# Kernel optimization log

Measured on AMD Instinct MI355X. Metric: run time of the kernel, lower is better.

Reference implementation:

```python
import jax, jax.numpy as jnp
import numpy as np

N_NODES = 50000
N_EDGES = 800000
IN_CH, HID, OUT_CH = 3, 64, 768
NEG_SLOPE = 0.01  # torch LeakyReLU default
BN_EPS = 1e-5


def _gcn_conv(x, edge_index, W, b):
    # PyG GCNConv: add self-loops, symmetric degree normalization, scatter-add.
    n = x.shape[0]
    loops = jnp.arange(n, dtype=edge_index.dtype)
    src = jnp.concatenate([edge_index[0], loops])
    dst = jnp.concatenate([edge_index[1], loops])
    deg = jax.ops.segment_sum(jnp.ones(src.shape[0], x.dtype), dst, num_segments=n)
    dinv = jnp.where(deg > 0, jax.lax.rsqrt(deg), 0.0)
    norm = dinv[src] * dinv[dst]                      # [E+N]
    h = x @ W                                          # [N, out]
    msg = h[src] * norm[:, None]                       # gather + edge scale
    return jax.ops.segment_sum(msg, dst, num_segments=n) + b


def _block(x, edge_index, W, b, gamma, beta):
    h = _gcn_conv(x, edge_index, W, b)
    h = jnp.where(h >= 0, h, NEG_SLOPE * h)            # LeakyReLU
    mean = h.mean(axis=0)
    var = h.var(axis=0)                                # biased, as torch BN train
    h = (h - mean) * jax.lax.rsqrt(var + BN_EPS) * gamma + beta
    return h                                           # dropout: identity (eval)


def _glorot(key, fan_in, fan_out):
    s = np.sqrt(6.0 / (fan_in + fan_out)).astype(np.float32)
    return jax.random.uniform(key, (fan_in, fan_out), jnp.float32, -s, s)


def setup_inputs() -> dict:
    key = jax.random.key(0)
    ks = jax.random.split(key, 8)
    x = jax.random.normal(ks[0], (N_NODES, IN_CH), jnp.float32)
    edge_index = jax.random.randint(ks[1], (2, N_EDGES), 0, N_NODES, jnp.int64)
    inp = {"x": x, "edge_index": edge_index}
    inp["W1"] = _glorot(ks[2], IN_CH, HID)
    inp["b1"] = jnp.zeros((HID,), jnp.float32)
    inp["g1"] = jnp.ones((HID,), jnp.float32)
    inp["be1"] = jnp.zeros((HID,), jnp.float32)
    inp["W2"] = _glorot(ks[3], HID, HID)
    inp["b2"] = jnp.zeros((HID,), jnp.float32)
    inp["g2"] = jnp.ones((HID,), jnp.float32)
    inp["be2"] = jnp.zeros((HID,), jnp.float32)
    inp["W3"] = _glorot(ks[4], HID, HID)
    inp["b3"] = jnp.zeros((HID,), jnp.float32)
    inp["g3"] = jnp.ones((HID,), jnp.float32)
    inp["be3"] = jnp.zeros((HID,), jnp.float32)
    inp["Wmu"] = _glorot(ks[5], HID, OUT_CH)
    inp["bmu"] = jnp.zeros((OUT_CH,), jnp.float32)
    inp["Wls"] = _glorot(ks[6], HID, OUT_CH)
    inp["bls"] = jnp.zeros((OUT_CH,), jnp.float32)
    return inp


def reference(x, edge_index, W1, b1, g1, be1, W2, b2, g2, be2, W3, b3, g3, be3, Wmu, bmu, Wls, bls):
    h = _block(x, edge_index, W1, b1, g1, be1)
    h = _block(h, edge_index, W2, b2, g2, be2)
    h = _block(h, edge_index, W3, b3, g3, be3)
    mu = _gcn_conv(h, edge_index, Wmu, bmu)
    logstd = _gcn_conv(h, edge_index, Wls, bls)
    return (mu, logstd)
```

## Files before the change

### kernel.cpp

```cpp
#include <hip/hip_runtime.h>
#include <cstddef>


#define NEG_SLOPE 0.01f
#define BN_EPS 1e-5f

typedef unsigned short u16;
typedef __attribute__((ext_vector_type(8))) short bf16x8;
typedef __attribute__((ext_vector_type(4))) float f32x4;

__device__ __forceinline__ unsigned bf16_rne(float x) {
  unsigned u = __float_as_uint(x);
  return (u + 0x7fffu + ((u >> 16) & 1u)) >> 16;
}

__global__ __launch_bounds__(256) void init_k(int* __restrict__ cnt,
                                              float* __restrict__ bns, int N) {
  int i = blockIdx.x * 256 + threadIdx.x;
  if (i < N) cnt[i] = 0;
  if (i < 384) bns[i] = 0.0f;
}

__global__ __launch_bounds__(256) void hist_k(const int* __restrict__ dst,
                                              int* __restrict__ cnt, int E) {
  int e = blockIdx.x * 256 + threadIdx.x;
  if (e < E) atomicAdd(&cnt[dst[e]], 1);
}

__global__ __launch_bounds__(1024) void scanA(const int* __restrict__ cnt,
                                              int* __restrict__ pre,
                                              int* __restrict__ bsum, int N) {
  __shared__ int sh[1024];
  const int t = threadIdx.x;
  const int i = blockIdx.x * 1024 + t;
  int c = (i < N) ? cnt[i] : 0;
  sh[t] = c;
  __syncthreads();
  for (int off = 1; off < 1024; off <<= 1) {
    int v = (t >= off) ? sh[t - off] : 0;
    __syncthreads();
    sh[t] += v;
    __syncthreads();
  }
  if (i < N) pre[i] = sh[t] - c;
  if (t == 1023) bsum[blockIdx.x] = sh[t];
}

__global__ __launch_bounds__(64) void scanB(int* __restrict__ bsum, int nb) {
  int t = threadIdx.x;
  int orig = (t < nb) ? bsum[t] : 0;
  int v = orig;
#pragma unroll
  for (int off = 1; off < 64; off <<= 1) {
    int u = __shfl_up(v, off);
    if (t >= off) v += u;
  }
  if (t < nb) bsum[t] = v - orig;
}

__global__ __launch_bounds__(256) void scanC(const int* __restrict__ cnt,
                                             int* __restrict__ rowptr,
                                             int* __restrict__ cursor,
                                             const int* __restrict__ bsum,
                                             const float* __restrict__ x,
                                             float* __restrict__ dinv,
                                             float4* __restrict__ xd,
                                             int N, int E) {
  int i = blockIdx.x * 256 + threadIdx.x;
  if (i < N) {
    int rp = rowptr[i] + bsum[i >> 10];
    rowptr[i] = rp;
    cursor[i] = rp;
    float dv = rsqrtf((float)(cnt[i] + 1));
    dinv[i] = dv;
    xd[i] = make_float4(x[i * 3] * dv, x[i * 3 + 1] * dv, x[i * 3 + 2] * dv, dv);
  }
  if (i == 0) rowptr[N] = E;
}

__global__ __launch_bounds__(256) void fill_k(const int* __restrict__ src,
                                              const int* __restrict__ dst,
                                              int* __restrict__ cursor,
                                              int* __restrict__ eidx, int E) {
  int e = blockIdx.x * 256 + threadIdx.x;
  if (e >= E) return;
  int p = atomicAdd(&cursor[dst[e]], 1);
  eidx[p] = src[e];
}

__global__ __launch_bounds__(256) void l1_fused(
    const int* __restrict__ rowptr, const int* __restrict__ eidx,
    const float4* __restrict__ xd, const float* __restrict__ W1,
    const float* __restrict__ b1, float* __restrict__ Z, float* __restrict__ q,
    float* __restrict__ bns, int N) {
  const int t = threadIdx.x, lane = t & 63, wid = t >> 6;
  const int gw = blockIdx.x * 4 + wid;
  const int nw = gridDim.x * 4;
  const float w0 = W1[lane], w1 = W1[64 + lane], w2 = W1[128 + lane];
  const float bb = b1[lane];
  float s1 = 0.f, s2 = 0.f;
  for (int node = gw; node < N; node += nw) {
    int beg = rowptr[node], end = rowptr[node + 1];
    float a0 = 0.f, a1 = 0.f, a2 = 0.f, aq = 0.f;
    for (int e = beg + lane; e < end; e += 64) {
      float4 v = xd[eidx[e]];
      a0 += v.x;
      a1 += v.y;
      a2 += v.z;
      aq += v.w;
    }
#pragma unroll
    for (int off = 32; off; off >>= 1) {
      a0 += __shfl_xor(a0, off);
      a1 += __shfl_xor(a1, off);
      a2 += __shfl_xor(a2, off);
      aq += __shfl_xor(aq, off);
    }
    float4 sv = xd[node];
    float dv = sv.w;
    a0 += sv.x;
    a1 += sv.y;
    a2 += sv.z;
    aq += dv;
    float u = dv * (a0 * w0 + a1 * w1 + a2 * w2) + bb;
    float o = u >= 0.f ? u : NEG_SLOPE * u;
    Z[(size_t)node * 64 + lane] = o * dv;
    s1 += o;
    s2 += o * o;
    if (lane == 0) q[node] = aq;
  }
  __shared__ float red[8][64];
  red[wid][lane] = s1;
  red[4 + wid][lane] = s2;
  __syncthreads();
  if (t < 64) {
    atomicAdd(&bns[t], red[0][t] + red[1][t] + red[2][t] + red[3][t]);
    atomicAdd(&bns[64 + t], red[4][t] + red[5][t] + red[6][t] + red[7][t]);
  }
}

__global__ __launch_bounds__(256) void gather64(const int* __restrict__ rowptr,
                                                const int* __restrict__ eidx,
                                                const float* __restrict__ Z,
                                                float* __restrict__ G, int N) {
  int node = blockIdx.x * 4 + (threadIdx.x >> 6);
  if (node >= N) return;
  int lane = threadIdx.x & 63;
  int slot = lane >> 4;
  int c4 = (lane & 15) << 2;
  int beg = rowptr[node], end = rowptr[node + 1];
  float ax = 0.f, ay = 0.f, az = 0.f, aw = 0.f;
  int e = beg + slot;
  for (; e + 4 < end; e += 8) {
    int s0 = eidx[e], s1 = eidx[e + 4];
    float4 v0 = *(const float4*)(Z + (size_t)s0 * 64 + c4);
    float4 v1 = *(const float4*)(Z + (size_t)s1 * 64 + c4);
    ax += v0.x + v1.x;
    ay += v0.y + v1.y;
    az += v0.z + v1.z;
    aw += v0.w + v1.w;
  }
  if (e < end) {
    int s0 = eidx[e];
    float4 v0 = *(const float4*)(Z + (size_t)s0 * 64 + c4);
    ax += v0.x; ay += v0.y; az += v0.z; aw += v0.w;
  }
#pragma unroll
  for (int off = 16; off < 64; off <<= 1) {
    ax += __shfl_xor(ax, off);
    ay += __shfl_xor(ay, off);
    az += __shfl_xor(az, off);
    aw += __shfl_xor(aw, off);
  }
  if (slot == 0) {
    float4 self = *(const float4*)(Z + (size_t)node * 64 + c4);
    float4 o = make_float4(ax + self.x, ay + self.y, az + self.z, aw + self.w);
    *(float4*)(G + (size_t)node * 64 + c4) = o;
  }
}

__global__ __launch_bounds__(256) void gather64h(const int* __restrict__ rowptr,
                                                 const int* __restrict__ eidx,
                                                 const float* __restrict__ Z,
                                                 u16* __restrict__ Ghi,
                                                 u16* __restrict__ Glo, int N) {
  int node = blockIdx.x * 4 + (threadIdx.x >> 6);
  if (node >= N) return;
  int lane = threadIdx.x & 63;
  int slot = lane >> 4;
  int c4 = (lane & 15) << 2;
  int beg = rowptr[node], end = rowptr[node + 1];
  float ax = 0.f, ay = 0.f, az = 0.f, aw = 0.f;
  int e = beg + slot;
  for (; e + 4 < end; e += 8) {
    int s0 = eidx[e], s1 = eidx[e + 4];
    float4 v0 = *(const float4*)(Z + (size_t)s0 * 64 + c4);
    float4 v1 = *(const float4*)(Z + (size_t)s1 * 64 + c4);
    ax += v0.x + v1.x;
    ay += v0.y + v1.y;
    az += v0.z + v1.z;
    aw += v0.w + v1.w;
  }
  if (e < end) {
    int s0 = eidx[e];
    float4 v0 = *(const float4*)(Z + (size_t)s0 * 64 + c4);
    ax += v0.x; ay += v0.y; az += v0.z; aw += v0.w;
  }
#pragma unroll
  for (int off = 16; off < 64; off <<= 1) {
    ax += __shfl_xor(ax, off);
    ay += __shfl_xor(ay, off);
    az += __shfl_xor(az, off);
    aw += __shfl_xor(aw, off);
  }
  if (slot == 0) {
    float4 self = *(const float4*)(Z + (size_t)node * 64 + c4);
    float o0 = ax + self.x, o1 = ay + self.y, o2 = az + self.z, o3 = aw + self.w;
    unsigned h0 = bf16_rne(o0), h1 = bf16_rne(o1), h2 = bf16_rne(o2), h3 = bf16_rne(o3);
    unsigned l0 = bf16_rne(o0 - __uint_as_float(h0 << 16));
    unsigned l1 = bf16_rne(o1 - __uint_as_float(h1 << 16));
    unsigned l2 = bf16_rne(o2 - __uint_as_float(h2 << 16));
    unsigned l3 = bf16_rne(o3 - __uint_as_float(h3 << 16));
    uint2 hv = make_uint2(h0 | (h1 << 16), h2 | (h3 << 16));
    uint2 lv = make_uint2(l0 | (l1 << 16), l2 | (l3 << 16));
    *(uint2*)(Ghi + (size_t)node * 64 + c4) = hv;
    *(uint2*)(Glo + (size_t)node * 64 + c4) = lv;
  }
}

__global__ __launch_bounds__(256) void prep_head(
    const float* __restrict__ bns, const float* __restrict__ g,
    const float* __restrict__ be, const float* __restrict__ Wmu,
    const float* __restrict__ Wls, u16* __restrict__ Bh, u16* __restrict__ Bl,
    float* __restrict__ cmu, float* __restrict__ cls, float invN) {
  __shared__ float sc[64], sh[64], part[2][128];
  int t = threadIdx.x;
  if (t < 64) {
    float mean = bns[t] * invN;
    float var = bns[64 + t] * invN - mean * mean;
    float s = g[t] * rsqrtf(var + BN_EPS);
    sc[t] = s;
    sh[t] = be[t] - mean * s;
  }
  __syncthreads();
  int blk = blockIdx.x;
  int head = blk >= 6 ? 1 : 0;
  int cc = head ? blk - 6 : blk;
  int c0 = cc * 128;
  const float* W = head ? Wls : Wmu;
  float* cx = head ? cls : cmu;
  int cl = t & 127, kh = t >> 7;
  int c = c0 + cl;
  int ct = cl >> 4, jc = cl & 15;
  size_t base = (size_t)(head * 6 + cc) * 2 * 8 * 64 * 8;
  float p = 0.f;
  for (int k = kh * 32; k < kh * 32 + 32; ++k) {
    float w = W[(size_t)k * 768 + c];
    float wc = sc[k] * w;
    p += sh[k] * w;
    unsigned hi = bf16_rne(wc);
    unsigned lo = bf16_rne(wc - __uint_as_float(hi << 16));
    int lane = ((k >> 3) & 3) * 16 + jc;
    size_t idx = base + (((size_t)kh * 8 + ct) * 64 + lane) * 8 + (k & 7);
    Bh[idx] = (u16)hi;
    Bl[idx] = (u16)lo;
  }
  part[kh][cl] = p;
  __syncthreads();
  if (t < 128) cx[c0 + t] = part[0][t] + part[1][t];
}

__global__ __launch_bounds__(256, 4) void gemm_bnq2(
    const float* __restrict__ G, const float* __restrict__ dinv,
    const float* __restrict__ q, const float* __restrict__ W,
    const float* __restrict__ g, const float* __restrict__ be,
    const float* __restrict__ bnsPrev, const float* __restrict__ b,
    float* __restrict__ Z, float* __restrict__ bnsOut, float invN, int N) {
  __shared__ __align__(16) float P[64][68];
  __shared__ __align__(16) float Ws[64][64];
  __shared__ float scl[64], shl[64], cxl[64], part[4][64];
  const int t = threadIdx.x;
  const int r0 = blockIdx.x * 64;

  if (t < 64) {
    float mean = bnsPrev[t] * invN;
    float var = bnsPrev[64 + t] * invN - mean * mean;
    float s = g[t] * rsqrtf(var + BN_EPS);
    scl[t] = s;
    shl[t] = be[t] - mean * s;
  }
  for (int i = t; i < 1024; i += 256) {
    int r = i >> 4, k4 = (i & 15) << 2, gr = r0 + r;
    float4 v = make_float4(0.f, 0.f, 0.f, 0.f);
    if (gr < N) v = *(const float4*)(G + (size_t)gr * 64 + k4);
    *(float4*)&P[r][k4] = v;
  }
  for (int i = t; i < 4096; i += 256) Ws[i >> 6][i & 63] = W[i];
  __syncthreads();

  {
    const int c = t & 63, k0 = t >> 6;
    float p = 0.f;
#pragma unroll
    for (int s = 0; s < 16; ++s) {
      int k = k0 + (s << 2);
      float w = Ws[k][c];
      Ws[k][c] = scl[k] * w;
      p += shl[k] * w;
    }
    part[k0][c] = p;
  }
  __syncthreads();
  if (t < 64) cxl[t] = part[0][t] + part[1][t] + part[2][t] + part[3][t];
  __syncthreads();

  const int tr = t >> 4, tc4 = (t & 15) << 2;
  float acc[4][4] = {};
#pragma unroll 8
  for (int k = 0; k < 64; ++k) {
    float4 w = *(const float4*)&Ws[k][tc4];
#pragma unroll
    for (int i = 0; i < 4; ++i) {
      float a = P[tr + 16 * i][k];
      acc[i][0] += a * w.x;
      acc[i][1] += a * w.y;
      acc[i][2] += a * w.z;
      acc[i][3] += a * w.w;
    }
  }

  float s1[4] = {0.f, 0.f, 0.f, 0.f}, s2[4] = {0.f, 0.f, 0.f, 0.f};
  float4 bb = *(const float4*)(b + tc4);
  float4 cc = make_float4(cxl[tc4], cxl[tc4 + 1], cxl[tc4 + 2], cxl[tc4 + 3]);
#pragma unroll
  for (int i = 0; i < 4; ++i) {
    int r = r0 + tr + 16 * i;
    if (r < N) {
      float dv = dinv[r];
      float dq = dv * q[r];
      float u0 = acc[i][0] * dv + dq * cc.x + bb.x;
      float u1 = acc[i][1] * dv + dq * cc.y + bb.y;
      float u2 = acc[i][2] * dv + dq * cc.z + bb.z;
      float u3 = acc[i][3] * dv + dq * cc.w + bb.w;
      float o0 = u0 >= 0.f ? u0 : NEG_SLOPE * u0;
      float o1 = u1 >= 0.f ? u1 : NEG_SLOPE * u1;
      float o2 = u2 >= 0.f ? u2 : NEG_SLOPE * u2;
      float o3 = u3 >= 0.f ? u3 : NEG_SLOPE * u3;
      float4 z = make_float4(o0 * dv, o1 * dv, o2 * dv, o3 * dv);
      *(float4*)(Z + (size_t)r * 64 + tc4) = z;
      s1[0] += o0; s2[0] += o0 * o0;
      s1[1] += o1; s2[1] += o1 * o1;
      s1[2] += o2; s2[2] += o2 * o2;
      s1[3] += o3; s2[3] += o3 * o3;
    }
  }
  __syncthreads();
  float (*red1)[64] = (float(*)[64]) & Ws[0][0];
  float (*red2)[64] = (float(*)[64]) & Ws[16][0];
#pragma unroll
  for (int j = 0; j < 4; ++j) {
    red1[tr][tc4 + j] = s1[j];
    red2[tr][tc4 + j] = s2[j];
  }
  __syncthreads();
  if (t < 64) {
    float a1 = 0.f, a2 = 0.f;
#pragma unroll
    for (int i = 0; i < 16; ++i) {
      a1 += red1[i][t];
      a2 += red2[i][t];
    }
    atomicAdd(&bnsOut[t], a1);
    atomicAdd(&bnsOut[64 + t], a2);
  }
}

__global__ __launch_bounds__(256) void head_mfma2(
    const u16* __restrict__ Ghi, const u16* __restrict__ Glo,
    const float* __restrict__ dinv, const float* __restrict__ q,
    const u16* __restrict__ Bh, const u16* __restrict__ Bl,
    const float* __restrict__ cmu, const float* __restrict__ bmu,
    const float* __restrict__ cls, const float* __restrict__ bls,
    float* __restrict__ OUT, int N, int ntiles) {
  const int t = threadIdx.x;
  const int w = t >> 6, l = t & 63;
  const int yy = blockIdx.y;
  const int head = (yy >= 6) ? 1 : 0;
  const int cc = head ? yy - 6 : yy;
  const int c0 = cc * 128;
  const float* cx = head ? cls : cmu;
  const float* bb = head ? bls : bmu;
  float* O = OUT + (head ? (size_t)N * 768 : 0);

  const size_t base = (size_t)(head * 6 + cc) * 2 * 8 * 64 * 8;
  const u16* bhp = Bh + base;
  const u16* blp = Bl + base;
  bf16x8 wh[8][2], wl[8][2];
#pragma unroll
  for (int ct = 0; ct < 8; ++ct) {
    wh[ct][0] = *(const bf16x8*)(bhp + (((size_t)ct) * 64 + l) * 8);
    wh[ct][1] = *(const bf16x8*)(bhp + (((size_t)(8 + ct)) * 64 + l) * 8);
    wl[ct][0] = *(const bf16x8*)(blp + (((size_t)ct) * 64 + l) * 8);
    wl[ct][1] = *(const bf16x8*)(blp + (((size_t)(8 + ct)) * 64 + l) * 8);
  }

  const int colb = c0 + ((l >> 4) << 2);
  for (int tile = blockIdx.x; tile < ntiles; tile += gridDim.x) {
    const int grow = tile * 64 + w * 16 + (l & 15);
    const int gc = grow < N ? grow : N - 1;
    const u16* gh = Ghi + (size_t)gc * 64 + ((l >> 4) << 3);
    const u16* gl = Glo + (size_t)gc * 64 + ((l >> 4) << 3);
    const bf16x8 gh0 = *(const bf16x8*)gh;
    const bf16x8 gh1 = *(const bf16x8*)(gh + 32);
    const bf16x8 gl0 = *(const bf16x8*)gl;
    const bf16x8 gl1 = *(const bf16x8*)(gl + 32);
    const float dv = dinv[gc];
    const float dq = dv * q[gc];

#pragma unroll
    for (int ct = 0; ct < 8; ++ct) {
      f32x4 a = {0.f, 0.f, 0.f, 0.f};
      a = __builtin_amdgcn_mfma_f32_16x16x32_bf16(wh[ct][0], gh0, a, 0, 0, 0);
      a = __builtin_amdgcn_mfma_f32_16x16x32_bf16(wh[ct][1], gh1, a, 0, 0, 0);
      a = __builtin_amdgcn_mfma_f32_16x16x32_bf16(wl[ct][0], gh0, a, 0, 0, 0);
      a = __builtin_amdgcn_mfma_f32_16x16x32_bf16(wl[ct][1], gh1, a, 0, 0, 0);
      a = __builtin_amdgcn_mfma_f32_16x16x32_bf16(wh[ct][0], gl0, a, 0, 0, 0);
      a = __builtin_amdgcn_mfma_f32_16x16x32_bf16(wh[ct][1], gl1, a, 0, 0, 0);
      if (grow < N) {
        int col = colb + ct * 16;
        float4 cxv = *(const float4*)(cx + col);
        float4 bbv = *(const float4*)(bb + col);
        float4 o = make_float4(a[0] * dv + dq * cxv.x + bbv.x,
                               a[1] * dv + dq * cxv.y + bbv.y,
                               a[2] * dv + dq * cxv.z + bbv.z,
                               a[3] * dv + dq * cxv.w + bbv.w);
        *(float4*)(O + (size_t)grow * 768 + col) = o;
      }
    }
  }
}

extern "C" void kernel_launch(void* const* d_in, const int* in_sizes, int n_in,
                              void* d_out, int out_size, void* d_ws, size_t ws_size,
                              hipStream_t stream) {
  const float* x   = (const float*)d_in[0];
  const int*   ei  = (const int*)d_in[1];
  const float* W1  = (const float*)d_in[2];
  const float* b1  = (const float*)d_in[3];
  const float* g1  = (const float*)d_in[4];
  const float* be1 = (const float*)d_in[5];
  const float* W2  = (const float*)d_in[6];
  const float* b2  = (const float*)d_in[7];
  const float* g2  = (const float*)d_in[8];
  const float* be2 = (const float*)d_in[9];
  const float* W3  = (const float*)d_in[10];
  const float* b3  = (const float*)d_in[11];
  const float* g3  = (const float*)d_in[12];
  const float* be3 = (const float*)d_in[13];
  const float* Wmu = (const float*)d_in[14];
  const float* bmu = (const float*)d_in[15];
  const float* Wls = (const float*)d_in[16];
  const float* bls = (const float*)d_in[17];

  const int N = in_sizes[0] / 3;
  const int E = in_sizes[1] / 2;
  const int* src = ei;
  const int* dst = ei + E;
  float* out = (float*)d_out;

  char* ws = (char*)d_ws;
  size_t o = 0;
  float* dinv = (float*)(ws + o); o += (size_t)N * 4;
  float* qv   = (float*)(ws + o); o += (size_t)N * 4;
  float* bns  = (float*)(ws + o); o += 384 * 4;
  float4* xd  = (float4*)(ws + o); o += (size_t)N * 16;
  u16* Bh     = (u16*)(ws + o);   o += (size_t)12 * 2 * 8 * 64 * 8 * 2;
  u16* Bl     = (u16*)(ws + o);   o += (size_t)12 * 2 * 8 * 64 * 8 * 2;
  float* cmu  = (float*)(ws + o); o += 768 * 4;
  float* cls  = (float*)(ws + o); o += 768 * 4;
  u16* Ghi    = (u16*)(ws + o);   o += (size_t)N * 64 * 2;
  u16* Glo    = (u16*)(ws + o);   o += (size_t)N * 64 * 2;
  int* cnt    = (int*)(ws + o);   o += (size_t)N * 4;
  int* rowptr = (int*)(ws + o);   o += ((size_t)N + 1) * 4;
  int* cursor = (int*)(ws + o);   o += (size_t)N * 4;
  int* bsum   = (int*)(ws + o);   o += 64 * 4;
  int* eidx   = (int*)(ws + o);   o += (size_t)E * 4;
  float* B0   = (float*)(ws + o); o += (size_t)N * 64 * 4;
  float* B1   = (float*)(ws + o); o += (size_t)N * 64 * 4;

  const float invN = 1.0f / (float)N;
  int nbN = (N + 255) / 256;
  int nbE = (E + 255) / 256;
  int gb  = (N + 63) / 64;
  int wb  = (N + 3) / 4;
  int sbA = (N + 1023) / 1024;

  init_k<<<nbN, 256, 0, stream>>>(cnt, bns, N);
  hist_k<<<nbE, 256, 0, stream>>>(dst, cnt, E);
  scanA<<<sbA, 1024, 0, stream>>>(cnt, rowptr, bsum, N);
  scanB<<<1, 64, 0, stream>>>(bsum, sbA);
  scanC<<<nbN, 256, 0, stream>>>(cnt, rowptr, cursor, bsum, x, dinv, xd, N, E);
  fill_k<<<nbE, 256, 0, stream>>>(src, dst, cursor, eidx, E);

  l1_fused<<<1024, 256, 0, stream>>>(rowptr, eidx, xd, W1, b1, B0, qv, bns, N);

  gather64<<<wb, 256, 0, stream>>>(rowptr, eidx, B0, B1, N);
  gemm_bnq2<<<gb, 256, 0, stream>>>(B1, dinv, qv, W2, g1, be1, bns + 0, b2,
                                    B0, bns + 128, invN, N);

  gather64<<<wb, 256, 0, stream>>>(rowptr, eidx, B0, B1, N);
  gemm_bnq2<<<gb, 256, 0, stream>>>(B1, dinv, qv, W3, g2, be2, bns + 128, b3,
                                    B0, bns + 256, invN, N);
  prep_head<<<12, 256, 0, stream>>>(bns + 256, g3, be3, Wmu, Wls, Bh, Bl, cmu, cls, invN);

  gather64h<<<wb, 256, 0, stream>>>(rowptr, eidx, B0, Ghi, Glo, N);
  dim3 hgrid(64, 12);
  head_mfma2<<<hgrid, 256, 0, stream>>>(Ghi, Glo, dinv, qv, Bh, Bl,
                                        cmu, bmu, cls, bls, out, N, gb);
}
```

Baseline: 417.9 us.

## Swap head kernel loop order: one block per row tile, stream weight chunks

The head GEMM kernel no longer pins one 128-column weight chunk in registers per block and loops over row tiles. Each block now owns one 64-row tile, loads its gathered activations once, and iterates over all 12 column chunks, loading weight fragments from global or L2 inside the loop. This cuts register pressure and reuses the activation loads across both heads. In exchange, weight fragments are re-read from cache by every block, and the grid grows from 768 persistent blocks to one per row tile.

```diff
diff --git a/kernel.cpp b/kernel.cpp
--- a/kernel.cpp
+++ b/kernel.cpp
@@ -375,59 +375,54 @@
   }
 }
 
-__global__ __launch_bounds__(256) void head_mfma2(
+__global__ __launch_bounds__(256) void head_mfma3(
     const u16* __restrict__ Ghi, const u16* __restrict__ Glo,
     const float* __restrict__ dinv, const float* __restrict__ q,
     const u16* __restrict__ Bh, const u16* __restrict__ Bl,
     const float* __restrict__ cmu, const float* __restrict__ bmu,
     const float* __restrict__ cls, const float* __restrict__ bls,
-    float* __restrict__ OUT, int N, int ntiles) {
+    float* __restrict__ OUT, int N) {
   const int t = threadIdx.x;
   const int w = t >> 6, l = t & 63;
-  const int yy = blockIdx.y;
-  const int head = (yy >= 6) ? 1 : 0;
-  const int cc = head ? yy - 6 : yy;
-  const int c0 = cc * 128;
-  const float* cx = head ? cls : cmu;
-  const float* bb = head ? bls : bmu;
-  float* O = OUT + (head ? (size_t)N * 768 : 0);
-
-  const size_t base = (size_t)(head * 6 + cc) * 2 * 8 * 64 * 8;
-  const u16* bhp = Bh + base;
-  const u16* blp = Bl + base;
-  bf16x8 wh[8][2], wl[8][2];
-#pragma unroll
-  for (int ct = 0; ct < 8; ++ct) {
-    wh[ct][0] = *(const bf16x8*)(bhp + (((size_t)ct) * 64 + l) * 8);
-    wh[ct][1] = *(const bf16x8*)(bhp + (((size_t)(8 + ct)) * 64 + l) * 8);
-    wl[ct][0] = *(const bf16x8*)(blp + (((size_t)ct) * 64 + l) * 8);
-    wl[ct][1] = *(const bf16x8*)(blp + (((size_t)(8 + ct)) * 64 + l) * 8);
-  }
-
-  const int colb = c0 + ((l >> 4) << 2);
-  for (int tile = blockIdx.x; tile < ntiles; tile += gridDim.x) {
-    const int grow = tile * 64 + w * 16 + (l & 15);
-    const int gc = grow < N ? grow : N - 1;
-    const u16* gh = Ghi + (size_t)gc * 64 + ((l >> 4) << 3);
-    const u16* gl = Glo + (size_t)gc * 64 + ((l >> 4) << 3);
-    const bf16x8 gh0 = *(const bf16x8*)gh;
-    const bf16x8 gh1 = *(const bf16x8*)(gh + 32);
-    const bf16x8 gl0 = *(const bf16x8*)gl;
-    const bf16x8 gl1 = *(const bf16x8*)(gl + 32);
-    const float dv = dinv[gc];
-    const float dq = dv * q[gc];
-
-#pragma unroll
+  const int grow = blockIdx.x * 64 + w * 16 + (l & 15);
+  const int gc = grow < N ? grow : N - 1;
+
+  const u16* gh = Ghi + (size_t)gc * 64 + ((l >> 4) << 3);
+  const u16* gl = Glo + (size_t)gc * 64 + ((l >> 4) << 3);
+  const bf16x8 gh0 = *(const bf16x8*)gh;
+  const bf16x8 gh1 = *(const bf16x8*)(gh + 32);
+  const bf16x8 gl0 = *(const bf16x8*)gl;
+  const bf16x8 gl1 = *(const bf16x8*)(gl + 32);
+  const float dv = dinv[gc];
+  const float dq = dv * q[gc];
+  const int colq = (l >> 4) << 2;
+
+  for (int chunk = 0; chunk < 12; ++chunk) {
+    const int head = (chunk >= 6) ? 1 : 0;
+    const int cc = head ? chunk - 6 : chunk;
+    const int c0 = cc * 128;
+    const float* cx = head ? cls : cmu;
+    const float* bb = head ? bls : bmu;
+    float* O = OUT + (head ? (size_t)N * 768 : 0);
+    const size_t base = (size_t)chunk * 2 * 8 * 64 * 8;
+    const u16* bhp = Bh + base;
+    const u16* blp = Bl + base;
+
+#pragma unroll 2
     for (int ct = 0; ct < 8; ++ct) {
+      const bf16x8 wh0 = *(const bf16x8*)(bhp + (((size_t)ct) * 64 + l) * 8);
+      const bf16x8 wh1 = *(const bf16x8*)(bhp + (((size_t)(8 + ct)) * 64 + l) * 8);
+      const bf16x8 wl0 = *(const bf16x8*)(blp + (((size_t)ct) * 64 + l) * 8);
+      const bf16x8 wl1 = *(const bf16x8*)(blp + (((size_t)(8 + ct)) * 64 + l) * 8);
       f32x4 a = {0.f, 0.f, 0.f, 0.f};
-      a = __builtin_amdgcn_mfma_f32_16x16x32_bf16(wh[ct][0], gh0, a, 0, 0, 0);
-      a = __builtin_amdgcn_mfma_f32_16x16x32_bf16(wh[ct][1], gh1, a, 0, 0, 0);
-      a = __builtin_amdgcn_mfma_f32_16x16x32_bf16(wl[ct][0], gh0, a, 0, 0, 0);
-      a = __builtin_amdgcn_mfma_f32_16x16x32_bf16(wl[ct][1], gh1, a, 0, 0, 0);
-      a = __builtin_amdgcn_mfma_f32_16x16x32_bf16(wh[ct][0], gl0, a, 0, 0, 0);
-      a = __builtin_amdgcn_mfma_f32_16x16x32_bf16(wh[ct][1], gl1, a, 0, 0, 0);
+      a = __builtin_amdgcn_mfma_f32_16x16x32_bf16(wh0, gh0, a, 0, 0, 0);
+      a = __builtin_amdgcn_mfma_f32_16x16x32_bf16(wh1, gh1, a, 0, 0, 0);
+      a = __builtin_amdgcn_mfma_f32_16x16x32_bf16(wl0, gh0, a, 0, 0, 0);
+      a = __builtin_amdgcn_mfma_f32_16x16x32_bf16(wl1, gh1, a, 0, 0, 0);
+      a = __builtin_amdgcn_mfma_f32_16x16x32_bf16(wh0, gl0, a, 0, 0, 0);
+      a = __builtin_amdgcn_mfma_f32_16x16x32_bf16(wh1, gl1, a, 0, 0, 0);
       if (grow < N) {
-        int col = colb + ct * 16;
+        int col = c0 + colq + ct * 16;
         float4 cxv = *(const float4*)(cx + col);
         float4 bbv = *(const float4*)(bb + col);
         float4 o = make_float4(a[0] * dv + dq * cxv.x + bbv.x,
@@ -514,7 +509,6 @@
   prep_head<<<12, 256, 0, stream>>>(bns + 256, g3, be3, Wmu, Wls, Bh, Bl, cmu, cls, invN);
 
   gather64h<<<wb, 256, 0, stream>>>(rowptr, eidx, B0, Ghi, Glo, N);
-  dim3 hgrid(64, 12);
-  head_mfma2<<<hgrid, 256, 0, stream>>>(Ghi, Glo, dinv, qv, Bh, Bl,
-                                        cmu, bmu, cls, bls, out, N, gb);
-}
+  head_mfma3<<<gb, 256, 0, stream>>>(Ghi, Glo, dinv, qv, Bh, Bl,
+                                     cmu, bmu, cls, bls, out, N);
+}
```

After: 446.0 us. 1.07x slower.
